# Optimization experiments

Hardware: AMD Instinct MI355X
Metric: run time of the kernel (lower is better)

The kernel has to match this reference:

```python
import jax, jax.numpy as jnp
import numpy as np

# Dims inferred from the module: conv weight (K=3, C_IN=C+1, C_OUT=C)
K_W = 3
C_OUT = 64
C_IN = C_OUT + 1
B, L = 32, 8192
N_STEPS = 8  # fixed-step RK4 stand-in for odeint(rtol=atol=1e-3) over t in [0,1]


def setup_inputs() -> dict:
    key = jax.random.key(0)
    kx, kw = jax.random.split(key)
    x = jax.random.normal(kx, (B, L, C_OUT), dtype=jnp.float32)
    # lecun_uniform: U(-sqrt(3/fan_in), sqrt(3/fan_in)), fan_in = K_W * C_IN
    limit = float(np.sqrt(3.0 / (K_W * C_IN)))
    w = jax.random.uniform(kw, (K_W, C_IN, C_OUT), dtype=jnp.float32,
                           minval=-limit, maxval=limit)
    b = jnp.zeros((C_OUT,), dtype=jnp.float32)
    return {"x": x, "w": w, "b": b}


def _ode_func(y, t, w, b):
    # concat_t: append a constant-t channel -> (B, L, C+1)
    t_chan = jnp.full(y.shape[:-1] + (1,), 1.0, dtype=y.dtype) * t
    z = jnp.concatenate([y, t_chan], axis=-1)
    z = jax.lax.conv_general_dilated(
        z, w, window_strides=(1,), padding="SAME",
        dimension_numbers=("NWC", "WIO", "NWC"))
    return jax.nn.relu(z + b)


def reference(x, w, b):
    h = jnp.float32(1.0 / N_STEPS)

    def step(y, t0):
        k1 = _ode_func(y, t0, w, b)
        k2 = _ode_func(y + 0.5 * h * k1, t0 + 0.5 * h, w, b)
        k3 = _ode_func(y + 0.5 * h * k2, t0 + 0.5 * h, w, b)
        k4 = _ode_func(y + h * k3, t0 + h, w, b)
        y_next = y + (h / 6.0) * (k1 + 2.0 * k2 + 2.0 * k3 + k4)
        return y_next, None

    ts = jnp.arange(N_STEPS, dtype=jnp.float32) * h
    y_final, _ = jax.lax.scan(step, x, ts)
    return y_final
```

## Files before the change

kernel.cpp:

```cpp
#include <hip/hip_runtime.h>


#define BB 32
#define LL 8192
#define CC 64
#define HALO 8
#define TILE 80
#define NBLK 103
#define CROWS 96
#define BUFR 98
#define ZST 72
#define THREADS 256

typedef __attribute__((ext_vector_type(8))) short bf16x8;
typedef __attribute__((ext_vector_type(4))) float f32x4;

__device__ __forceinline__ unsigned bf_rne(float f) {
    unsigned u = __float_as_uint(f);
    return u + 0x7fffu + ((u >> 16) & 1u);
}
__device__ __forceinline__ short bf16_of(float f) { return (short)(bf_rne(f) >> 16); }
__device__ __forceinline__ unsigned cvtpk(float lo, float hi) {
    unsigned r;
    asm("v_cvt_pk_bf16_f32 %0, %1, %2" : "=v"(r) : "v"(lo), "v"(hi));
    return r;
}

__launch_bounds__(THREADS, 3)
__global__ void step_kernel(const float* __restrict__ y_in, float* __restrict__ y_out,
                            const float* __restrict__ w, const float* __restrict__ bias,
                            float t0, float h)
{
    __shared__ unsigned short zA[BUFR * ZST];
    __shared__ unsigned short zB[BUFR * ZST];

    const int tid = threadIdx.x;
    const int b = blockIdx.y;
    const int l0 = blockIdx.x * TILE;
    const int lane = tid & 63;
    const int wv = tid >> 6;
    const int ch = wv & 1;
    const int rh = wv >> 1;
    const int g = lane >> 4;
    const int ml = lane & 15;
    const int co = ch * 32 + 2 * ml;
    const bool edge = (blockIdx.x == 0) || (blockIdx.x == NBLK - 1);

    const int rmin = (blockIdx.x == 0) ? HALO : 0;
    const int rmax = min(CROWS, LL - l0 + HALO);

    if (tid < 64) {
        zA[tid] = 0; zA[(BUFR - 1) * ZST + tid] = 0;
        zB[tid] = 0; zB[(BUFR - 1) * ZST + tid] = 0;
    }

    bf16x8 Bf[6][2];
#pragma unroll
    for (int c = 0; c < 6; c++) {
        const float* wp = w + (c >> 1) * (65 * CC) + (((c & 1) * 32) + g * 8) * CC + co;
#pragma unroll
        for (int j = 0; j < 8; j++) {
            float2 v = *(const float2*)(wp + j * CC);
            Bf[c][0][j] = bf16_of(v.x);
            Bf[c][1][j] = bf16_of(v.y);
        }
    }
    const float2 wt0 = *(const float2*)(w + 0 * (65 * CC) + CC * CC + co);
    const float2 wt1 = *(const float2*)(w + 1 * (65 * CC) + CC * CC + co);
    const float2 wt2 = *(const float2*)(w + 2 * (65 * CC) + CC * CC + co);
    const float2 bv  = *(const float2*)(bias + co);

    const float* yrow = y_in + ((size_t)b * LL + (size_t)(l0 - HALO)) * CC;
    for (int idx = tid; idx < CROWS * 16; idx += THREADS) {
        const int row = idx >> 4;
        const int c4 = (idx & 15) * 4;
        float4 v = make_float4(0.f, 0.f, 0.f, 0.f);
        if (row >= rmin && row < rmax)
            v = *(const float4*)(yrow + (size_t)row * CC + c4);
        uint2 p;
        p.x = cvtpk(v.x, v.y);
        p.y = cvtpk(v.z, v.w);
        *(uint2*)&zA[(row + 1) * ZST + c4] = p;
    }

    float2 yR[3][4];
#pragma unroll
    for (int bb = 0; bb < 3; bb++) {
#pragma unroll
        for (int i = 0; i < 4; i++) {
            const int r = (rh * 3 + bb) * 16 + g * 4 + i;
            float2 v = make_float2(0.f, 0.f);
            if (r >= rmin && r < rmax)
                v = *(const float2*)(y_in + ((size_t)b * LL + (size_t)(l0 - HALO + r)) * CC + co);
            yR[bb][i] = v;
        }
    }
    __syncthreads();

    float2 aR[3][4];
    const float ca[4]  = {h / 6.f, h / 3.f, h / 3.f, h / 6.f};
    const float cuv[4] = {0.5f * h, 0.5f * h, h, 0.f};
    const float tof[4] = {0.f, 0.5f * h, 0.5f * h, h};

#pragma unroll 1
    for (int e4 = 0; e4 < 8; e4++) {
        const int e = e4 & 3;
        const unsigned short* zin = (e4 & 1) ? zB : zA;
        unsigned short* zout = (e4 & 1) ? zA : zB;
        const float t = t0 + ((e4 >> 2) ? h : 0.f) + tof[e];
        const float cacc = ca[e], cuu = cuv[e];
        const float2 tb = {t * (wt0.x + wt1.x + wt2.x) + bv.x,
                           t * (wt0.y + wt1.y + wt2.y) + bv.y};

#pragma unroll
        for (int bb = 0; bb < 3; bb++) {
            const int r0 = (rh * 3 + bb) * 16;
            f32x4 acc0 = {0.f, 0.f, 0.f, 0.f};
            f32x4 acc1 = {0.f, 0.f, 0.f, 0.f};
#pragma unroll
            for (int c = 0; c < 6; c++) {
                const int zr = r0 + ml + (c >> 1);
                const bf16x8 a =
                    *(const bf16x8*)&zin[zr * ZST + ((c & 1) * 32) + g * 8];
                acc0 = __builtin_amdgcn_mfma_f32_16x16x32_bf16(a, Bf[c][0], acc0, 0, 0, 0);
                acc1 = __builtin_amdgcn_mfma_f32_16x16x32_bf16(a, Bf[c][1], acc1, 0, 0, 0);
            }
#pragma unroll
            for (int i = 0; i < 4; i++) {
                const int r = r0 + g * 4 + i;
                float k0 = acc0[i] + tb.x;
                float k1 = acc1[i] + tb.y;
                if (edge) {
                    const int l = l0 - HALO + r;
                    if (l == 0)      { k0 -= t * wt0.x; k1 -= t * wt0.y; }
                    if (l == LL - 1) { k0 -= t * wt2.x; k1 -= t * wt2.y; }
                }
                k0 = fmaxf(k0, 0.f);
                k1 = fmaxf(k1, 0.f);
                const float2 y2 = yR[bb][i];
                if (e == 0) {
                    aR[bb][i].x = y2.x + cacc * k0;
                    aR[bb][i].y = y2.y + cacc * k1;
                } else {
                    aR[bb][i].x += cacc * k0;
                    aR[bb][i].y += cacc * k1;
                }
                if (e4 == 3)
                    yR[bb][i] = aR[bb][i];
                if (e4 != 7) {
                    float u0 = 0.f, u1 = 0.f;
                    if (r >= rmin && r < rmax) {
                        if (e == 3) { u0 = yR[bb][i].x; u1 = yR[bb][i].y; }
                        else        { u0 = y2.x + cuu * k0; u1 = y2.y + cuu * k1; }
                    }
                    *(unsigned*)&zout[(r + 1) * ZST + co] = cvtpk(u0, u1);
                }
            }
        }
        if (e4 != 7) __syncthreads();
    }

#pragma unroll
    for (int bb = 0; bb < 3; bb++) {
        const int r0 = (rh * 3 + bb) * 16;
#pragma unroll
        for (int i = 0; i < 4; i++) {
            const int r = r0 + g * 4 + i;
            if (r >= HALO && r < HALO + TILE && r < rmax) {
                const int l = l0 - HALO + r;
                *(float2*)(y_out + ((size_t)b * LL + l) * CC + co) = aR[bb][i];
            }
        }
    }
}

extern "C" void kernel_launch(void* const* d_in, const int* in_sizes, int n_in,
                              void* d_out, int out_size, void* d_ws, size_t ws_size,
                              hipStream_t stream) {
    const float* x = (const float*)d_in[0];
    const float* w = (const float*)d_in[1];
    const float* bias = (const float*)d_in[2];
    float* out = (float*)d_out;
    float* P0 = (float*)d_ws;
    const float h = 1.0f / 8.0f;

    dim3 grid(NBLK, BB), block(THREADS);
    for (int s = 0; s < 4; s++) {
        const float* yin = (s == 0) ? x : ((s & 1) ? P0 : out);
        float* yout = (s & 1) ? out : P0;
        step_kernel<<<grid, block, 0, stream>>>(yin, yout, w, bias, (2 * s) * h, h);
    }
}
```

Before: 685.3 us.

## Swizzle LDS activation tiles and vectorize RK4 epilogue with packed float2 math

Applies an XOR swizzle (flipping the 32-column half on alternate groups of eight rows) to the bf16 activation buffers in shared memory, consistently for the initial fill, the MFMA A-operand reads and the stage writes. The aim is to cut LDS bank conflicts on the 16-byte fragment reads and the 4-byte stores. It also rewrites the per-element RK4 update with two-wide float vectors so the compiler can emit packed FP32 ops. Both change instruction mix and addressing without changing the maths, but the swizzle adds XOR address arithmetic.

```diff
diff --git a/kernel.cpp b/kernel.cpp
--- a/kernel.cpp
+++ b/kernel.cpp
@@ -12,8 +12,11 @@
 #define ZST 72
 #define THREADS 256
 
+#define SW(zr) ((((zr) >> 3) & 1) << 5)
+
 typedef __attribute__((ext_vector_type(8))) short bf16x8;
 typedef __attribute__((ext_vector_type(4))) float f32x4;
+typedef __attribute__((ext_vector_type(2))) float f32x2;
 
 __device__ __forceinline__ unsigned bf_rne(float f) {
     unsigned u = __float_as_uint(f);
@@ -80,24 +83,24 @@
         uint2 p;
         p.x = cvtpk(v.x, v.y);
         p.y = cvtpk(v.z, v.w);
-        *(uint2*)&zA[(row + 1) * ZST + c4] = p;
+        *(uint2*)&zA[(row + 1) * ZST + (c4 ^ SW(row + 1))] = p;
     }
 
-    float2 yR[3][4];
+    f32x2 yR[3][4];
 #pragma unroll
     for (int bb = 0; bb < 3; bb++) {
 #pragma unroll
         for (int i = 0; i < 4; i++) {
             const int r = (rh * 3 + bb) * 16 + g * 4 + i;
-            float2 v = make_float2(0.f, 0.f);
+            f32x2 v = {0.f, 0.f};
             if (r >= rmin && r < rmax)
-                v = *(const float2*)(y_in + ((size_t)b * LL + (size_t)(l0 - HALO + r)) * CC + co);
+                v = *(const f32x2*)(y_in + ((size_t)b * LL + (size_t)(l0 - HALO + r)) * CC + co);
             yR[bb][i] = v;
         }
     }
     __syncthreads();
 
-    float2 aR[3][4];
+    f32x2 aR[3][4];
     const float ca[4]  = {h / 6.f, h / 3.f, h / 3.f, h / 6.f};
     const float cuv[4] = {0.5f * h, 0.5f * h, h, 0.f};
     const float tof[4] = {0.f, 0.5f * h, 0.5f * h, h};
@@ -109,7 +112,7 @@
         unsigned short* zout = (e4 & 1) ? zA : zB;
         const float t = t0 + ((e4 >> 2) ? h : 0.f) + tof[e];
         const float cacc = ca[e], cuu = cuv[e];
-        const float2 tb = {t * (wt0.x + wt1.x + wt2.x) + bv.x,
+        const f32x2 tb2 = {t * (wt0.x + wt1.x + wt2.x) + bv.x,
                            t * (wt0.y + wt1.y + wt2.y) + bv.y};
 
 #pragma unroll
@@ -120,40 +123,33 @@
 #pragma unroll
             for (int c = 0; c < 6; c++) {
                 const int zr = r0 + ml + (c >> 1);
-                const bf16x8 a =
-                    *(const bf16x8*)&zin[zr * ZST + ((c & 1) * 32) + g * 8];
+                const int off = zr * ZST + ((((c & 1) * 32) + g * 8) ^ SW(zr));
+                const bf16x8 a = *(const bf16x8*)&zin[off];
                 acc0 = __builtin_amdgcn_mfma_f32_16x16x32_bf16(a, Bf[c][0], acc0, 0, 0, 0);
                 acc1 = __builtin_amdgcn_mfma_f32_16x16x32_bf16(a, Bf[c][1], acc1, 0, 0, 0);
             }
 #pragma unroll
             for (int i = 0; i < 4; i++) {
                 const int r = r0 + g * 4 + i;
-                float k0 = acc0[i] + tb.x;
-                float k1 = acc1[i] + tb.y;
+                f32x2 k = {acc0[i], acc1[i]};
+                k += tb2;
                 if (edge) {
                     const int l = l0 - HALO + r;
-                    if (l == 0)      { k0 -= t * wt0.x; k1 -= t * wt0.y; }
-                    if (l == LL - 1) { k0 -= t * wt2.x; k1 -= t * wt2.y; }
+                    if (l == 0)      { k.x -= t * wt0.x; k.y -= t * wt0.y; }
+                    if (l == LL - 1) { k.x -= t * wt2.x; k.y -= t * wt2.y; }
                 }
-                k0 = fmaxf(k0, 0.f);
-                k1 = fmaxf(k1, 0.f);
-                const float2 y2 = yR[bb][i];
-                if (e == 0) {
-                    aR[bb][i].x = y2.x + cacc * k0;
-                    aR[bb][i].y = y2.y + cacc * k1;
-                } else {
-                    aR[bb][i].x += cacc * k0;
-                    aR[bb][i].y += cacc * k1;
-                }
+                k = __builtin_elementwise_max(k, (f32x2){0.f, 0.f});
+                const f32x2 y2 = yR[bb][i];
+                if (e == 0) aR[bb][i] = y2 + cacc * k;
+                else        aR[bb][i] = aR[bb][i] + cacc * k;
                 if (e4 == 3)
                     yR[bb][i] = aR[bb][i];
                 if (e4 != 7) {
-                    float u0 = 0.f, u1 = 0.f;
+                    f32x2 u = {0.f, 0.f};
                     if (r >= rmin && r < rmax) {
-                        if (e == 3) { u0 = yR[bb][i].x; u1 = yR[bb][i].y; }
-                        else        { u0 = y2.x + cuu * k0; u1 = y2.y + cuu * k1; }
+                        u = (e == 3) ? yR[bb][i] : (y2 + cuu * k);
                     }
-                    *(unsigned*)&zout[(r + 1) * ZST + co] = cvtpk(u0, u1);
+                    *(unsigned*)&zout[(r + 1) * ZST + (co ^ SW(r + 1))] = cvtpk(u.x, u.y);
                 }
             }
         }
@@ -168,7 +164,7 @@
             const int r = r0 + g * 4 + i;
             if (r >= HALO && r < HALO + TILE && r < rmax) {
                 const int l = l0 - HALO + r;
-                *(float2*)(y_out + ((size_t)b * LL + l) * CC + co) = aR[bb][i];
+                *(f32x2*)(y_out + ((size_t)b * LL + l) * CC + co) = aR[bb][i];
             }
         }
     }
```

After: 918.3 us. 1.34x slower.
